# Kernel tuning notes

Measured on AMD Instinct MI355X. Metric: run time of the kernel, lower is better.

Reference implementation:

```python
import jax, jax.numpy as jnp
import numpy as np

N_NODES = 170000
N_EDGES = 1200000
IN, HID, OUT = 128, 128, 64


def setup_inputs() -> dict:
    key = jax.random.key(0)
    ks = jax.random.split(key, 9)
    feat = jax.random.normal(ks[0], (N_NODES, IN), dtype=jnp.float32)
    src = jax.random.randint(ks[1], (N_EDGES,), 0, N_NODES, dtype=jnp.int32)
    dst = jax.random.randint(ks[2], (N_EDGES,), 0, N_NODES, dtype=jnp.int32)
    # Glorot-uniform style init for the GraphConv weights, zero bias (DGL default)
    def glorot(k, fan_in, fan_out):
        lim = np.sqrt(6.0 / (fan_in + fan_out)).astype(np.float32)
        return jax.random.uniform(k, (fan_in, fan_out), jnp.float32, -lim, lim)
    W0 = glorot(ks[3], IN, HID)
    W1 = glorot(ks[4], HID, HID)
    W2 = glorot(ks[5], HID, OUT)
    b0 = jnp.zeros((HID,), jnp.float32)
    b1 = jnp.zeros((HID,), jnp.float32)
    b2 = jnp.zeros((OUT,), jnp.float32)
    return {"feat": feat, "src": src, "dst": dst,
            "W0": W0, "b0": b0, "W1": W1, "b1": b1, "W2": W2, "b2": b2}


def _gcn_layer(h, src, dst, norm_out, norm_in, W, b, relu):
    # norm='both': D_out^{-1/2} scaling, sum-aggregate over edges, D_in^{-1/2} scaling
    h = h * norm_out                                   # [N, d]
    agg = jax.ops.segment_sum(h[src], dst, num_segments=N_NODES)  # gather+scatter-add
    r = (agg * norm_in) @ W + b                        # dense transform + bias
    return jax.nn.relu(r) if relu else r


def reference(feat, src, dst, W0, b0, W1, b1, W2, b2):
    ones = jnp.ones((N_EDGES,), jnp.float32)
    # DGL clamps degrees to min 1 (allow_zero_in_degree=True keeps zero-degree nodes)
    deg_out = jnp.clip(jax.ops.segment_sum(ones, src, num_segments=N_NODES), 1.0)
    deg_in = jnp.clip(jax.ops.segment_sum(ones, dst, num_segments=N_NODES), 1.0)
    norm_out = (deg_out ** -0.5)[:, None]
    norm_in = (deg_in ** -0.5)[:, None]
    # Dropout(0.5) between layers is identity in eval mode
    h = _gcn_layer(feat, src, dst, norm_out, norm_in, W0, b0, relu=True)
    h = _gcn_layer(h, src, dst, norm_out, norm_in, W1, b1, relu=True)
    h = _gcn_layer(h, src, dst, norm_out, norm_in, W2, b2, relu=False)
    return h
```

## Files before the change

kernel.cpp:

```cpp
#include <hip/hip_runtime.h>
#include <hip/hip_bf16.h>

#define N_NODES 170000
#define N_EDGES 1200000

#define AITEMS 2048
#define NB_A   586
#define NCB    333
#define SCAN_A_N      (NCB * NB_A)
#define SCAN_A_BLOCKS 191
#define SCAN_A_PAD    (SCAN_A_BLOCKS * 1024)
#define HISTA_PAD     195140

#define DOUT_NPC    16384
#define DOUT_WPC    8192
#define DOUT_NCHUNK 11
#define DOUT_NSLICE 96
#define DOUT_SLICE_E (N_EDGES / DOUT_NSLICE)
#define WORDS_N     85000

typedef short bf16x8 __attribute__((ext_vector_type(8)));
typedef float f32x4 __attribute__((ext_vector_type(4)));

__device__ __forceinline__ void bf_split(float v, __hip_bfloat16& h, __hip_bfloat16& l)
{
    h = __float2bfloat16(v);
    l = __float2bfloat16(v - __bfloat162float(h));
}


__global__ __launch_bounds__(256) void coarse_hist_kernel(
    const int* __restrict__ dst, int* __restrict__ histA, int nedges)
{
    __shared__ int h[NCB];
    int t = threadIdx.x;
    for (int j = t; j < NCB; j += 256) h[j] = 0;
    __syncthreads();
    int base = blockIdx.x * AITEMS;
    #pragma unroll
    for (int j = 0; j < AITEMS / 256; j++) {
        int i = base + j * 256 + t;
        if (i < nedges) atomicAdd(&h[dst[i] >> 9], 1);
    }
    __syncthreads();
    for (int j = t; j < NCB; j += 256)
        histA[j * NB_A + blockIdx.x] = h[j];
}

__global__ __launch_bounds__(256) void scan1_kernel(
    const int* __restrict__ in, int* __restrict__ partial,
    int* __restrict__ blockSums, int n)
{
    __shared__ int sdata[256];
    int t = threadIdx.x;
    int base = blockIdx.x * 1024 + t * 4;
    int4 v = make_int4(0, 0, 0, 0);
    if (base + 3 < n) v = *(const int4*)&in[base];
    else {
        if (base + 0 < n) v.x = in[base + 0];
        if (base + 1 < n) v.y = in[base + 1];
        if (base + 2 < n) v.z = in[base + 2];
        if (base + 3 < n) v.w = in[base + 3];
    }
    int tsum = v.x + v.y + v.z + v.w;
    sdata[t] = tsum;
    __syncthreads();
    for (int off = 1; off < 256; off <<= 1) {
        int add = 0;
        if (t >= off) add = sdata[t - off];
        __syncthreads();
        if (t >= off) sdata[t] += add;
        __syncthreads();
    }
    int excl = sdata[t] - tsum;
    int4 o;
    o.x = excl;
    o.y = o.x + v.x;
    o.z = o.y + v.y;
    o.w = o.z + v.z;
    *(int4*)&partial[base] = o;
    if (t == 255) blockSums[blockIdx.x] = sdata[255];
}

__global__ __launch_bounds__(256) void scan2_kernel(int* __restrict__ blockSums, int nb)
{
    __shared__ int sdata[256];
    int t = threadIdx.x;
    int val = (t < nb) ? blockSums[t] : 0;
    sdata[t] = val;
    __syncthreads();
    for (int off = 1; off < 256; off <<= 1) {
        int add = 0;
        if (t >= off) add = sdata[t - off];
        __syncthreads();
        if (t >= off) sdata[t] += add;
        __syncthreads();
    }
    if (t < nb) blockSums[t] = sdata[t] - val;
}

__global__ __launch_bounds__(256) void scan3_kernel(
    int* __restrict__ buf, const int* __restrict__ blockSums)
{
    int off = blockSums[blockIdx.x];
    int base = blockIdx.x * 1024 + threadIdx.x * 4;
    int4 v = *(const int4*)&buf[base];
    v.x += off; v.y += off; v.z += off; v.w += off;
    *(int4*)&buf[base] = v;
}

__global__ __launch_bounds__(256) void coarse_scatter_kernel(
    const int* __restrict__ src, const int* __restrict__ dst,
    const int* __restrict__ scanA, int* __restrict__ pairs, int nedges)
{
    __shared__ int base[NCB];
    __shared__ int cur[NCB];
    int t = threadIdx.x;
    for (int j = t; j < NCB; j += 256) {
        base[j] = scanA[j * NB_A + blockIdx.x];
        cur[j] = 0;
    }
    __syncthreads();
    int eb = blockIdx.x * AITEMS;
    #pragma unroll
    for (int j = 0; j < AITEMS / 256; j++) {
        int i = eb + j * 256 + t;
        if (i < nedges) {
            int d = dst[i];
            int cb = d >> 9;
            int r = atomicAdd(&cur[cb], 1);
            pairs[base[cb] + r] = (src[i] << 9) | (d & 511);
        }
    }
}

__global__ __launch_bounds__(256) void bucket_sort_kernel(
    const int* __restrict__ pairs, const int* __restrict__ scanA,
    int* __restrict__ csr, int* __restrict__ row_start,
    float* __restrict__ norm_in, int nedges)
{
    __shared__ int hist[512];
    __shared__ int curs[512];
    __shared__ int sdata[256];
    int cb = blockIdx.x;
    int t = threadIdx.x;
    int beg = scanA[cb * NB_A];
    int end = (cb == NCB - 1) ? nedges : scanA[(cb + 1) * NB_A];

    hist[t] = 0; hist[t + 256] = 0;
    __syncthreads();
    for (int j = beg + t; j < end; j += 256)
        atomicAdd(&hist[pairs[j] & 511], 1);
    __syncthreads();

    int a = hist[2 * t], b = hist[2 * t + 1];
    sdata[t] = a + b;
    __syncthreads();
    for (int off = 1; off < 256; off <<= 1) {
        int add = 0;
        if (t >= off) add = sdata[t - off];
        __syncthreads();
        if (t >= off) sdata[t] += add;
        __syncthreads();
    }
    int epair = sdata[t] - (a + b);
    curs[2 * t]     = beg + epair;
    curs[2 * t + 1] = beg + epair + a;
    __syncthreads();

    int nodeBase = cb << 9;
    for (int s = t; s < 512; s += 256) {
        int v = nodeBase + s;
        if (v < N_NODES) {
            row_start[v] = curs[s];
            norm_in[v] = rsqrtf(fmaxf((float)hist[s], 1.0f));
        }
    }
    if (cb == NCB - 1 && t == 0) row_start[N_NODES] = nedges;
    __syncthreads();

    for (int j = beg + t; j < end; j += 256) {
        int p = pairs[j];
        int pos = atomicAdd(&curs[p & 511], 1);
        csr[pos] = p >> 9;
    }
}

__global__ __launch_bounds__(256) void degout_hist_kernel(
    const int* __restrict__ src, unsigned* __restrict__ partial)
{
    __shared__ unsigned h[DOUT_WPC];
    int chunk = blockIdx.x / DOUT_NSLICE;
    int slice = blockIdx.x % DOUT_NSLICE;
    int lo = chunk * DOUT_NPC;
    int t = threadIdx.x;
    #pragma unroll
    for (int j = 0; j < DOUT_WPC / 256; j++) h[j * 256 + t] = 0;
    __syncthreads();
    const int4* sp = (const int4*)(src + slice * DOUT_SLICE_E);
    for (int i = t; i < DOUT_SLICE_E / 4; i += 256) {
        int4 v = sp[i];
        unsigned a = (unsigned)(v.x - lo);
        if (a < DOUT_NPC) atomicAdd(&h[a >> 1], 1u << ((a & 1) * 16));
        a = (unsigned)(v.y - lo);
        if (a < DOUT_NPC) atomicAdd(&h[a >> 1], 1u << ((a & 1) * 16));
        a = (unsigned)(v.z - lo);
        if (a < DOUT_NPC) atomicAdd(&h[a >> 1], 1u << ((a & 1) * 16));
        a = (unsigned)(v.w - lo);
        if (a < DOUT_NPC) atomicAdd(&h[a >> 1], 1u << ((a & 1) * 16));
    }
    __syncthreads();
    int wlo = chunk * DOUT_WPC;
    int nw = min(DOUT_WPC, WORDS_N - wlo);
    for (int j = t; j < nw; j += 256)
        partial[(size_t)slice * WORDS_N + wlo + j] = h[j];
}

__global__ __launch_bounds__(256) void degout_combine_kernel(
    const unsigned* __restrict__ partial, float* __restrict__ norm_out)
{
    int w = blockIdx.x * 256 + threadIdx.x;
    if (w >= WORDS_N) return;
    unsigned slo = 0, shi = 0;
    #pragma unroll
    for (int s = 0; s < DOUT_NSLICE; s++) {
        unsigned x = partial[(size_t)s * WORDS_N + w];
        slo += x & 0xFFFFu;
        shi += x >> 16;
    }
    norm_out[2 * w]     = rsqrtf(fmaxf((float)slo, 1.0f));
    norm_out[2 * w + 1] = rsqrtf(fmaxf((float)shi, 1.0f));
}

__global__ __launch_bounds__(256) void f2bf_kernel(
    const float* __restrict__ in, __hip_bfloat16* __restrict__ outp, int n8)
{
    int i = blockIdx.x * 256 + threadIdx.x;
    if (i >= n8) return;
    float4 a = *(const float4*)&in[(size_t)i * 8];
    float4 b = *(const float4*)&in[(size_t)i * 8 + 4];
    float4 packed;
    __hip_bfloat162* p = (__hip_bfloat162*)&packed;
    p[0].x = __float2bfloat16(a.x); p[0].y = __float2bfloat16(a.y);
    p[1].x = __float2bfloat16(a.z); p[1].y = __float2bfloat16(a.w);
    p[2].x = __float2bfloat16(b.x); p[2].y = __float2bfloat16(b.y);
    p[3].x = __float2bfloat16(b.z); p[3].y = __float2bfloat16(b.w);
    *(float4*)&outp[(size_t)i * 8] = packed;
}

__global__ __launch_bounds__(256) void wsplit_kernel(
    const float* __restrict__ W, int nout,
    __hip_bfloat16* __restrict__ Whi, __hip_bfloat16* __restrict__ Wlo)
{
    int i = blockIdx.x * 256 + threadIdx.x;
    if (i >= 128 * nout) return;
    int k = i / nout, n = i - k * nout;
    float v = W[i];
    __hip_bfloat16 h, l;
    bf_split(v, h, l);
    Whi[n * 128 + k] = h;
    Wlo[n * 128 + k] = l;
}

template<int W, bool SCALE_SRC, bool SPLIT_OUT, bool BIAS>
__global__ __launch_bounds__(256) void gather_kernel(
    const __hip_bfloat16* __restrict__ h, const int* __restrict__ csr,
    const int* __restrict__ row_start, const float* __restrict__ norm_out,
    const float* __restrict__ norm_in, const float* __restrict__ bias,
    float* __restrict__ outf, __hip_bfloat16* __restrict__ ohi,
    __hip_bfloat16* __restrict__ olo)
{
    int tid = blockIdx.x * 256 + threadIdx.x;
    int row = tid >> 4;
    int l = threadIdx.x & 15;
    int gbase = threadIdx.x & 48;
    if (row >= N_NODES) return;
    int beg = row_start[row];
    int end = row_start[row + 1];
    float acc[8] = {};
    for (int j = beg; j < end; j += 16) {
        int cnt = min(16, end - j);
        int sv = 0;
        float nv = 0.f;
        if (j + l < end) {
            sv = csr[j + l];
            if (SCALE_SRC) nv = norm_out[sv];
        }
        for (int i = 0; i < cnt; i++) {
            int s = __shfl(sv, gbase + i);
            if (W == 128) {
                float4 raw = *(const float4*)(h + (size_t)s * 128 + l * 8);
                const __hip_bfloat162* pp = (const __hip_bfloat162*)&raw;
                float2 f0 = __bfloat1622float2(pp[0]);
                float2 f1 = __bfloat1622float2(pp[1]);
                float2 f2 = __bfloat1622float2(pp[2]);
                float2 f3 = __bfloat1622float2(pp[3]);
                if (SCALE_SRC) {
                    float sc = __shfl(nv, gbase + i);
                    acc[0] += f0.x * sc; acc[1] += f0.y * sc;
                    acc[2] += f1.x * sc; acc[3] += f1.y * sc;
                    acc[4] += f2.x * sc; acc[5] += f2.y * sc;
                    acc[6] += f3.x * sc; acc[7] += f3.y * sc;
                } else {
                    acc[0] += f0.x; acc[1] += f0.y;
                    acc[2] += f1.x; acc[3] += f1.y;
                    acc[4] += f2.x; acc[5] += f2.y;
                    acc[6] += f3.x; acc[7] += f3.y;
                }
            } else {
                float2 raw = *(const float2*)(h + (size_t)s * 64 + l * 4);
                const __hip_bfloat162* pp = (const __hip_bfloat162*)&raw;
                float2 f0 = __bfloat1622float2(pp[0]);
                float2 f1 = __bfloat1622float2(pp[1]);
                acc[0] += f0.x; acc[1] += f0.y;
                acc[2] += f1.x; acc[3] += f1.y;
            }
        }
    }
    float ni = norm_in[row];
    if (W == 128 && SPLIT_OUT) {
        float4 ph, pl;
        __hip_bfloat16* hp = (__hip_bfloat16*)&ph;
        __hip_bfloat16* lp = (__hip_bfloat16*)&pl;
        #pragma unroll
        for (int j = 0; j < 8; j++) bf_split(acc[j] * ni, hp[j], lp[j]);
        *(float4*)(ohi + (size_t)row * 128 + l * 8) = ph;
        *(float4*)(olo + (size_t)row * 128 + l * 8) = pl;
    } else if (W == 64) {
        float4 o0 = make_float4(acc[0] * ni, acc[1] * ni, acc[2] * ni, acc[3] * ni);
        if (BIAS) {
            float4 b = *(const float4*)&bias[l * 4];
            o0.x += b.x; o0.y += b.y; o0.z += b.z; o0.w += b.w;
        }
        *(float4*)&outf[(size_t)row * 64 + l * 4] = o0;
    }
}

template<int NT, bool RELU, bool BIAS, bool RS, bool SPLIT_OUT>
__global__ __launch_bounds__(256) void mfma_matmul_kernel(
    const __hip_bfloat16* __restrict__ Ahi, const __hip_bfloat16* __restrict__ Alo,
    const __hip_bfloat16* __restrict__ Wthi, const __hip_bfloat16* __restrict__ Wtlo,
    const float* __restrict__ bias, const float* __restrict__ rowscale,
    __hip_bfloat16* __restrict__ outhi, __hip_bfloat16* __restrict__ outlo,
    int nrows)
{
    const int OUTW = NT * 16;
    const int wave = threadIdx.x >> 6;
    const int lane = threadIdx.x & 63;
    const int n = lane & 15;
    const int q = lane >> 4;
    const int r0 = blockIdx.x * 128 + wave * 32;
    if (r0 >= nrows) return;
    const bool t1 = (r0 + 16) < nrows;
    const size_t a0off = (size_t)(r0 + n) * 128 + q * 8;
    const size_t a1off = (size_t)(t1 ? (r0 + 16 + n) : (r0 + n)) * 128 + q * 8;
    const size_t bbase = (size_t)n * 128 + q * 8;

    f32x4 acc0[NT], acc1[NT];
    const f32x4 zero = {0.f, 0.f, 0.f, 0.f};
    #pragma unroll
    for (int ct = 0; ct < NT; ct++) { acc0[ct] = zero; acc1[ct] = zero; }

    #pragma unroll 1
    for (int kc = 0; kc < 4; kc++) {
        bf16x8 ah0 = *(const bf16x8*)(Ahi + a0off + kc * 32);
        bf16x8 al0 = *(const bf16x8*)(Alo + a0off + kc * 32);
        bf16x8 ah1 = *(const bf16x8*)(Ahi + a1off + kc * 32);
        bf16x8 al1 = *(const bf16x8*)(Alo + a1off + kc * 32);
        #pragma unroll
        for (int ct = 0; ct < NT; ct++) {
            bf16x8 bh = *(const bf16x8*)(Wthi + (size_t)ct * 2048 + bbase + kc * 32);
            bf16x8 bl = *(const bf16x8*)(Wtlo + (size_t)ct * 2048 + bbase + kc * 32);
            acc0[ct] = __builtin_amdgcn_mfma_f32_16x16x32_bf16(ah0, bh, acc0[ct], 0, 0, 0);
            acc0[ct] = __builtin_amdgcn_mfma_f32_16x16x32_bf16(al0, bh, acc0[ct], 0, 0, 0);
            acc0[ct] = __builtin_amdgcn_mfma_f32_16x16x32_bf16(ah0, bl, acc0[ct], 0, 0, 0);
            acc1[ct] = __builtin_amdgcn_mfma_f32_16x16x32_bf16(ah1, bh, acc1[ct], 0, 0, 0);
            acc1[ct] = __builtin_amdgcn_mfma_f32_16x16x32_bf16(al1, bh, acc1[ct], 0, 0, 0);
            acc1[ct] = __builtin_amdgcn_mfma_f32_16x16x32_bf16(ah1, bl, acc1[ct], 0, 0, 0);
        }
    }

    float bcol[NT];
    #pragma unroll
    for (int ct = 0; ct < NT; ct++) bcol[ct] = BIAS ? bias[ct * 16 + n] : 0.f;

    #pragma unroll
    for (int r = 0; r < 4; r++) {
        int grow = r0 + q * 4 + r;
        float rs = RS ? rowscale[grow] : 1.f;
        #pragma unroll
        for (int ct = 0; ct < NT; ct++) {
            float v = acc0[ct][r] + bcol[ct];
            if (RELU) v = fmaxf(v, 0.f);
            v *= rs;
            size_t o = (size_t)grow * OUTW + ct * 16 + n;
            if (SPLIT_OUT) {
                __hip_bfloat16 h, l;
                bf_split(v, h, l);
                outhi[o] = h; outlo[o] = l;
            } else {
                outhi[o] = __float2bfloat16(v);
            }
        }
    }
    if (t1) {
        #pragma unroll
        for (int r = 0; r < 4; r++) {
            int grow = r0 + 16 + q * 4 + r;
            float rs = RS ? rowscale[grow] : 1.f;
            #pragma unroll
            for (int ct = 0; ct < NT; ct++) {
                float v = acc1[ct][r] + bcol[ct];
                if (RELU) v = fmaxf(v, 0.f);
                v *= rs;
                size_t o = (size_t)grow * OUTW + ct * 16 + n;
                if (SPLIT_OUT) {
                    __hip_bfloat16 h, l;
                    bf_split(v, h, l);
                    outhi[o] = h; outlo[o] = l;
                } else {
                    outhi[o] = __float2bfloat16(v);
                }
            }
        }
    }
}

extern "C" void kernel_launch(void* const* d_in, const int* in_sizes, int n_in,
                              void* d_out, int out_size, void* d_ws, size_t ws_size,
                              hipStream_t stream)
{
    const float* feat = (const float*)d_in[0];
    const int* src    = (const int*)d_in[1];
    const int* dst    = (const int*)d_in[2];
    const float* W0   = (const float*)d_in[3];
    const float* b0   = (const float*)d_in[4];
    const float* W1   = (const float*)d_in[5];
    const float* b1   = (const float*)d_in[6];
    const float* W2   = (const float*)d_in[7];
    const float* b2   = (const float*)d_in[8];
    float* out = (float*)d_out;

    const int N = N_NODES;
    const int E = N_EDGES;

    char* ws = (char*)d_ws;
    float* norm_out = (float*)ws;
    float* norm_in  = norm_out + N;
    int* row_start  = (int*)(norm_in + N);
    int* csr        = row_start + 170004;
    __hip_bfloat16* Wt0hi = (__hip_bfloat16*)(csr + E);
    __hip_bfloat16* Wt0lo = Wt0hi + 16384;
    __hip_bfloat16* Wt1hi = Wt0lo + 16384;
    __hip_bfloat16* Wt1lo = Wt1hi + 16384;
    __hip_bfloat16* Wt2hi = Wt1lo + 16384;
    __hip_bfloat16* Wt2lo = Wt2hi + 8192;
    __hip_bfloat16* bfbuf = Wt2lo + 8192;
    __hip_bfloat16* Ahi   = bfbuf + (size_t)N * 128;
    __hip_bfloat16* Alo   = Ahi + (size_t)N * 128;
    int* histA          = (int*)Ahi;
    int* scanA          = histA + HISTA_PAD;
    int* blockSumsA     = scanA + SCAN_A_PAD + 4;
    unsigned* partial   = (unsigned*)(blockSumsA + 256);
    int* pairs          = (int*)Alo;

    degout_hist_kernel<<<DOUT_NCHUNK * DOUT_NSLICE, 256, 0, stream>>>(src, partial);
    degout_combine_kernel<<<(WORDS_N + 255) / 256, 256, 0, stream>>>(partial, norm_out);
    coarse_hist_kernel<<<NB_A, 256, 0, stream>>>(dst, histA, E);
    scan1_kernel<<<SCAN_A_BLOCKS, 256, 0, stream>>>(histA, scanA, blockSumsA, SCAN_A_N);
    scan2_kernel<<<1, 256, 0, stream>>>(blockSumsA, SCAN_A_BLOCKS);
    scan3_kernel<<<SCAN_A_BLOCKS, 256, 0, stream>>>(scanA, blockSumsA);
    coarse_scatter_kernel<<<NB_A, 256, 0, stream>>>(src, dst, scanA, pairs, E);
    bucket_sort_kernel<<<NCB, 256, 0, stream>>>(pairs, scanA, csr, row_start, norm_in, E);
    f2bf_kernel<<<(N * 16 + 255) / 256, 256, 0, stream>>>(feat, bfbuf, N * 16);
    wsplit_kernel<<<64, 256, 0, stream>>>(W0, 128, Wt0hi, Wt0lo);
    wsplit_kernel<<<64, 256, 0, stream>>>(W1, 128, Wt1hi, Wt1lo);
    wsplit_kernel<<<32, 256, 0, stream>>>(W2, 64, Wt2hi, Wt2lo);

    const int gatherBlocks = (N * 16 + 255) / 256;
    const int mmBlocks = (N + 127) / 128;

    gather_kernel<128, true, true, false><<<gatherBlocks, 256, 0, stream>>>(
        bfbuf, csr, row_start, norm_out, norm_in, nullptr, nullptr, Ahi, Alo);
    mfma_matmul_kernel<8, true, true, true, false><<<mmBlocks, 256, 0, stream>>>(
        Ahi, Alo, Wt0hi, Wt0lo, b0, norm_out, bfbuf, nullptr, N);

    gather_kernel<128, false, true, false><<<gatherBlocks, 256, 0, stream>>>(
        bfbuf, csr, row_start, nullptr, norm_in, nullptr, nullptr, Ahi, Alo);
    mfma_matmul_kernel<8, true, true, true, true><<<mmBlocks, 256, 0, stream>>>(
        Ahi, Alo, Wt1hi, Wt1lo, b1, norm_out, Ahi, Alo, N);

    mfma_matmul_kernel<4, false, false, false, false><<<mmBlocks, 256, 0, stream>>>(
        Ahi, Alo, Wt2hi, Wt2lo, nullptr, nullptr, bfbuf, nullptr, N);
    gather_kernel<64, false, false, true><<<gatherBlocks, 256, 0, stream>>>(
        bfbuf, csr, row_start, nullptr, norm_in, b2, out, nullptr, nullptr);
}
```

Baseline: 638.1 us.

## Fuse neighbor gather with MFMA transform per layer via swizzled LDS tiles

Introduces a fused kernel in which each 32-row block gathers and aggregates its neighbor features, writes the hi/lo bf16 split into swizzled shared memory, and runs the MFMA weight multiply from LDS. The second layer also applies the W2 projection in the same kernel. This removes the global round trips of the split Ahi/Alo intermediates and two kernel launches. In exchange each block holds 16KB of LDS and must finish its gather before the matmul starts, which may reduce occupancy and latency hiding. Weight tiles are now re-read per 32-row block rather than per 128 rows.

New measurement: 518.7 us. 18.7% less time.

```diff
diff --git a/kernel.cpp b/kernel.cpp
--- a/kernel.cpp
+++ b/kernel.cpp
@@ -26,6 +26,11 @@
 {
     h = __float2bfloat16(v);
     l = __float2bfloat16(v - __bfloat162float(h));
+}
+
+__device__ __forceinline__ int lds_addr(int row, int col)
+{
+    return (row * 256 + col * 2) ^ ((row & 7) << 4);
 }
 
 
@@ -260,6 +265,177 @@
     bf_split(v, h, l);
     Whi[n * 128 + k] = h;
     Wlo[n * 128 + k] = l;
+}
+
+template<bool SCALE_SRC, bool FUSE2>
+__global__ __launch_bounds__(256) void fused_layer_kernel(
+    const __hip_bfloat16* __restrict__ hin, const int* __restrict__ csr,
+    const int* __restrict__ row_start, const float* __restrict__ norm_out,
+    const float* __restrict__ norm_in, const __hip_bfloat16* __restrict__ Wthi,
+    const __hip_bfloat16* __restrict__ Wtlo, const float* __restrict__ bias,
+    const float* __restrict__ rowscale, const __hip_bfloat16* __restrict__ W2thi,
+    const __hip_bfloat16* __restrict__ W2tlo, __hip_bfloat16* __restrict__ outp)
+{
+    __shared__ __align__(16) unsigned char smem[16384];
+    const int r0 = blockIdx.x * 32;
+
+    {
+        const int g = threadIdx.x >> 4;
+        const int l = threadIdx.x & 15;
+        const int gbase = threadIdx.x & 48;
+        for (int rr = 0; rr < 2; rr++) {
+            const int lrow = g + rr * 16;
+            const int row = r0 + lrow;
+            float acc[8] = {};
+            if (row < N_NODES) {
+                int beg = row_start[row];
+                int end = row_start[row + 1];
+                for (int j = beg; j < end; j += 16) {
+                    int cnt = min(16, end - j);
+                    int sv = 0;
+                    float nv = 0.f;
+                    if (j + l < end) {
+                        sv = csr[j + l];
+                        if (SCALE_SRC) nv = norm_out[sv];
+                    }
+                    for (int i = 0; i < cnt; i++) {
+                        int s = __shfl(sv, gbase + i);
+                        float4 raw = *(const float4*)(hin + (size_t)s * 128 + l * 8);
+                        const __hip_bfloat162* pp = (const __hip_bfloat162*)&raw;
+                        float2 f0 = __bfloat1622float2(pp[0]);
+                        float2 f1 = __bfloat1622float2(pp[1]);
+                        float2 f2 = __bfloat1622float2(pp[2]);
+                        float2 f3 = __bfloat1622float2(pp[3]);
+                        if (SCALE_SRC) {
+                            float sc = __shfl(nv, gbase + i);
+                            acc[0] += f0.x * sc; acc[1] += f0.y * sc;
+                            acc[2] += f1.x * sc; acc[3] += f1.y * sc;
+                            acc[4] += f2.x * sc; acc[5] += f2.y * sc;
+                            acc[6] += f3.x * sc; acc[7] += f3.y * sc;
+                        } else {
+                            acc[0] += f0.x; acc[1] += f0.y;
+                            acc[2] += f1.x; acc[3] += f1.y;
+                            acc[4] += f2.x; acc[5] += f2.y;
+                            acc[6] += f3.x; acc[7] += f3.y;
+                        }
+                    }
+                }
+            }
+            float ni = (row < N_NODES) ? norm_in[row] : 0.f;
+            float4 ph, pl;
+            __hip_bfloat16* hp = (__hip_bfloat16*)&ph;
+            __hip_bfloat16* lp = (__hip_bfloat16*)&pl;
+            #pragma unroll
+            for (int jj = 0; jj < 8; jj++) bf_split(acc[jj] * ni, hp[jj], lp[jj]);
+            int off = lds_addr(lrow, l * 8);
+            *(float4*)(smem + off) = ph;
+            *(float4*)(smem + 8192 + off) = pl;
+        }
+    }
+    __syncthreads();
+
+    const int wave = threadIdx.x >> 6;
+    const int lane = threadIdx.x & 63;
+    const int n = lane & 15;
+    const int q = lane >> 4;
+    const size_t bbase = (size_t)n * 128 + q * 8;
+    const f32x4 zero = {0.f, 0.f, 0.f, 0.f};
+    f32x4 acc0[2], acc1[2];
+    acc0[0] = zero; acc0[1] = zero; acc1[0] = zero; acc1[1] = zero;
+
+    #pragma unroll 1
+    for (int kc = 0; kc < 4; kc++) {
+        const int a0 = lds_addr(n, q * 8 + kc * 32);
+        const int a1 = lds_addr(n + 16, q * 8 + kc * 32);
+        bf16x8 ah0 = *(const bf16x8*)(smem + a0);
+        bf16x8 al0 = *(const bf16x8*)(smem + 8192 + a0);
+        bf16x8 ah1 = *(const bf16x8*)(smem + a1);
+        bf16x8 al1 = *(const bf16x8*)(smem + 8192 + a1);
+        #pragma unroll
+        for (int c = 0; c < 2; c++) {
+            const int ct = wave * 2 + c;
+            bf16x8 bh = *(const bf16x8*)(Wthi + (size_t)ct * 2048 + bbase + kc * 32);
+            bf16x8 bl = *(const bf16x8*)(Wtlo + (size_t)ct * 2048 + bbase + kc * 32);
+            acc0[c] = __builtin_amdgcn_mfma_f32_16x16x32_bf16(ah0, bh, acc0[c], 0, 0, 0);
+            acc0[c] = __builtin_amdgcn_mfma_f32_16x16x32_bf16(al0, bh, acc0[c], 0, 0, 0);
+            acc0[c] = __builtin_amdgcn_mfma_f32_16x16x32_bf16(ah0, bl, acc0[c], 0, 0, 0);
+            acc1[c] = __builtin_amdgcn_mfma_f32_16x16x32_bf16(ah1, bh, acc1[c], 0, 0, 0);
+            acc1[c] = __builtin_amdgcn_mfma_f32_16x16x32_bf16(al1, bh, acc1[c], 0, 0, 0);
+            acc1[c] = __builtin_amdgcn_mfma_f32_16x16x32_bf16(ah1, bl, acc1[c], 0, 0, 0);
+        }
+    }
+
+    float bcol[2];
+    bcol[0] = bias[(wave * 2 + 0) * 16 + n];
+    bcol[1] = bias[(wave * 2 + 1) * 16 + n];
+
+    if (!FUSE2) {
+        #pragma unroll
+        for (int r = 0; r < 4; r++) {
+            int g0 = r0 + q * 4 + r;
+            int g1 = g0 + 16;
+            float rs0 = rowscale[min(g0, N_NODES - 1)];
+            float rs1 = rowscale[min(g1, N_NODES - 1)];
+            #pragma unroll
+            for (int c = 0; c < 2; c++) {
+                int col = (wave * 2 + c) * 16 + n;
+                float v0 = fmaxf(acc0[c][r] + bcol[c], 0.f) * rs0;
+                float v1 = fmaxf(acc1[c][r] + bcol[c], 0.f) * rs1;
+                if (g0 < N_NODES) outp[(size_t)g0 * 128 + col] = __float2bfloat16(v0);
+                if (g1 < N_NODES) outp[(size_t)g1 * 128 + col] = __float2bfloat16(v1);
+            }
+        }
+    } else {
+        __syncthreads();
+        #pragma unroll
+        for (int r = 0; r < 4; r++) {
+            int lr0 = q * 4 + r;
+            int lr1 = lr0 + 16;
+            float rs0 = rowscale[min(r0 + lr0, N_NODES - 1)];
+            float rs1 = rowscale[min(r0 + lr1, N_NODES - 1)];
+            #pragma unroll
+            for (int c = 0; c < 2; c++) {
+                int col = (wave * 2 + c) * 16 + n;
+                float v0 = fmaxf(acc0[c][r] + bcol[c], 0.f) * rs0;
+                float v1 = fmaxf(acc1[c][r] + bcol[c], 0.f) * rs1;
+                __hip_bfloat16 hh, ll;
+                bf_split(v0, hh, ll);
+                *(__hip_bfloat16*)(smem + lds_addr(lr0, col)) = hh;
+                *(__hip_bfloat16*)(smem + 8192 + lds_addr(lr0, col)) = ll;
+                bf_split(v1, hh, ll);
+                *(__hip_bfloat16*)(smem + lds_addr(lr1, col)) = hh;
+                *(__hip_bfloat16*)(smem + 8192 + lds_addr(lr1, col)) = ll;
+            }
+        }
+        __syncthreads();
+
+        f32x4 c0 = zero, c1 = zero;
+        #pragma unroll 1
+        for (int kc = 0; kc < 4; kc++) {
+            const int a0 = lds_addr(n, q * 8 + kc * 32);
+            const int a1 = lds_addr(n + 16, q * 8 + kc * 32);
+            bf16x8 ah0 = *(const bf16x8*)(smem + a0);
+            bf16x8 al0 = *(const bf16x8*)(smem + 8192 + a0);
+            bf16x8 ah1 = *(const bf16x8*)(smem + a1);
+            bf16x8 al1 = *(const bf16x8*)(smem + 8192 + a1);
+            bf16x8 bh = *(const bf16x8*)(W2thi + (size_t)wave * 2048 + bbase + kc * 32);
+            bf16x8 bl = *(const bf16x8*)(W2tlo + (size_t)wave * 2048 + bbase + kc * 32);
+            c0 = __builtin_amdgcn_mfma_f32_16x16x32_bf16(ah0, bh, c0, 0, 0, 0);
+            c0 = __builtin_amdgcn_mfma_f32_16x16x32_bf16(al0, bh, c0, 0, 0, 0);
+            c0 = __builtin_amdgcn_mfma_f32_16x16x32_bf16(ah0, bl, c0, 0, 0, 0);
+            c1 = __builtin_amdgcn_mfma_f32_16x16x32_bf16(ah1, bh, c1, 0, 0, 0);
+            c1 = __builtin_amdgcn_mfma_f32_16x16x32_bf16(al1, bh, c1, 0, 0, 0);
+            c1 = __builtin_amdgcn_mfma_f32_16x16x32_bf16(ah1, bl, c1, 0, 0, 0);
+        }
+        #pragma unroll
+        for (int r = 0; r < 4; r++) {
+            int g0 = r0 + q * 4 + r;
+            int g1 = g0 + 16;
+            int col = wave * 16 + n;
+            if (g0 < N_NODES) outp[(size_t)g0 * 64 + col] = __float2bfloat16(c0[r]);
+            if (g1 < N_NODES) outp[(size_t)g1 * 64 + col] = __float2bfloat16(c1[r]);
+        }
+    }
 }
 
 template<int W, bool SCALE_SRC, bool SPLIT_OUT, bool BIAS>
@@ -336,96 +512,6 @@
     }
 }
 
-template<int NT, bool RELU, bool BIAS, bool RS, bool SPLIT_OUT>
-__global__ __launch_bounds__(256) void mfma_matmul_kernel(
-    const __hip_bfloat16* __restrict__ Ahi, const __hip_bfloat16* __restrict__ Alo,
-    const __hip_bfloat16* __restrict__ Wthi, const __hip_bfloat16* __restrict__ Wtlo,
-    const float* __restrict__ bias, const float* __restrict__ rowscale,
-    __hip_bfloat16* __restrict__ outhi, __hip_bfloat16* __restrict__ outlo,
-    int nrows)
-{
-    const int OUTW = NT * 16;
-    const int wave = threadIdx.x >> 6;
-    const int lane = threadIdx.x & 63;
-    const int n = lane & 15;
-    const int q = lane >> 4;
-    const int r0 = blockIdx.x * 128 + wave * 32;
-    if (r0 >= nrows) return;
-    const bool t1 = (r0 + 16) < nrows;
-    const size_t a0off = (size_t)(r0 + n) * 128 + q * 8;
-    const size_t a1off = (size_t)(t1 ? (r0 + 16 + n) : (r0 + n)) * 128 + q * 8;
-    const size_t bbase = (size_t)n * 128 + q * 8;
-
-    f32x4 acc0[NT], acc1[NT];
-    const f32x4 zero = {0.f, 0.f, 0.f, 0.f};
-    #pragma unroll
-    for (int ct = 0; ct < NT; ct++) { acc0[ct] = zero; acc1[ct] = zero; }
-
-    #pragma unroll 1
-    for (int kc = 0; kc < 4; kc++) {
-        bf16x8 ah0 = *(const bf16x8*)(Ahi + a0off + kc * 32);
-        bf16x8 al0 = *(const bf16x8*)(Alo + a0off + kc * 32);
-        bf16x8 ah1 = *(const bf16x8*)(Ahi + a1off + kc * 32);
-        bf16x8 al1 = *(const bf16x8*)(Alo + a1off + kc * 32);
-        #pragma unroll
-        for (int ct = 0; ct < NT; ct++) {
-            bf16x8 bh = *(const bf16x8*)(Wthi + (size_t)ct * 2048 + bbase + kc * 32);
-            bf16x8 bl = *(const bf16x8*)(Wtlo + (size_t)ct * 2048 + bbase + kc * 32);
-            acc0[ct] = __builtin_amdgcn_mfma_f32_16x16x32_bf16(ah0, bh, acc0[ct], 0, 0, 0);
-            acc0[ct] = __builtin_amdgcn_mfma_f32_16x16x32_bf16(al0, bh, acc0[ct], 0, 0, 0);
-            acc0[ct] = __builtin_amdgcn_mfma_f32_16x16x32_bf16(ah0, bl, acc0[ct], 0, 0, 0);
-            acc1[ct] = __builtin_amdgcn_mfma_f32_16x16x32_bf16(ah1, bh, acc1[ct], 0, 0, 0);
-            acc1[ct] = __builtin_amdgcn_mfma_f32_16x16x32_bf16(al1, bh, acc1[ct], 0, 0, 0);
-            acc1[ct] = __builtin_amdgcn_mfma_f32_16x16x32_bf16(ah1, bl, acc1[ct], 0, 0, 0);
-        }
-    }
-
-    float bcol[NT];
-    #pragma unroll
-    for (int ct = 0; ct < NT; ct++) bcol[ct] = BIAS ? bias[ct * 16 + n] : 0.f;
-
-    #pragma unroll
-    for (int r = 0; r < 4; r++) {
-        int grow = r0 + q * 4 + r;
-        float rs = RS ? rowscale[grow] : 1.f;
-        #pragma unroll
-        for (int ct = 0; ct < NT; ct++) {
-            float v = acc0[ct][r] + bcol[ct];
-            if (RELU) v = fmaxf(v, 0.f);
-            v *= rs;
-            size_t o = (size_t)grow * OUTW + ct * 16 + n;
-            if (SPLIT_OUT) {
-                __hip_bfloat16 h, l;
-                bf_split(v, h, l);
-                outhi[o] = h; outlo[o] = l;
-            } else {
-                outhi[o] = __float2bfloat16(v);
-            }
-        }
-    }
-    if (t1) {
-        #pragma unroll
-        for (int r = 0; r < 4; r++) {
-            int grow = r0 + 16 + q * 4 + r;
-            float rs = RS ? rowscale[grow] : 1.f;
-            #pragma unroll
-            for (int ct = 0; ct < NT; ct++) {
-                float v = acc1[ct][r] + bcol[ct];
-                if (RELU) v = fmaxf(v, 0.f);
-                v *= rs;
-                size_t o = (size_t)grow * OUTW + ct * 16 + n;
-                if (SPLIT_OUT) {
-                    __hip_bfloat16 h, l;
-                    bf_split(v, h, l);
-                    outhi[o] = h; outlo[o] = l;
-                } else {
-                    outhi[o] = __float2bfloat16(v);
-                }
-            }
-        }
-    }
-}
-
 extern "C" void kernel_launch(void* const* d_in, const int* in_sizes, int n_in,
                               void* d_out, int out_size, void* d_ws, size_t ws_size,
                               hipStream_t stream)
@@ -456,13 +542,13 @@
     __hip_bfloat16* Wt2hi = Wt1lo + 16384;
     __hip_bfloat16* Wt2lo = Wt2hi + 8192;
     __hip_bfloat16* bfbuf = Wt2lo + 8192;
-    __hip_bfloat16* Ahi   = bfbuf + (size_t)N * 128;
-    __hip_bfloat16* Alo   = Ahi + (size_t)N * 128;
-    int* histA          = (int*)Ahi;
+    __hip_bfloat16* h1    = bfbuf + (size_t)N * 128;
+    __hip_bfloat16* aux   = h1 + (size_t)N * 128;
+    int* histA          = (int*)h1;
     int* scanA          = histA + HISTA_PAD;
     int* blockSumsA     = scanA + SCAN_A_PAD + 4;
     unsigned* partial   = (unsigned*)(blockSumsA + 256);
-    int* pairs          = (int*)Alo;
+    int* pairs          = (int*)aux;
 
     degout_hist_kernel<<<DOUT_NCHUNK * DOUT_NSLICE, 256, 0, stream>>>(src, partial);
     degout_combine_kernel<<<(WORDS_N + 255) / 256, 256, 0, stream>>>(partial, norm_out);
@@ -477,21 +563,17 @@
     wsplit_kernel<<<64, 256, 0, stream>>>(W1, 128, Wt1hi, Wt1lo);
     wsplit_kernel<<<32, 256, 0, stream>>>(W2, 64, Wt2hi, Wt2lo);
 
+    const int fusedBlocks = (N + 31) / 32;
     const int gatherBlocks = (N * 16 + 255) / 256;
-    const int mmBlocks = (N + 127) / 128;
-
-    gather_kernel<128, true, true, false><<<gatherBlocks, 256, 0, stream>>>(
-        bfbuf, csr, row_start, norm_out, norm_in, nullptr, nullptr, Ahi, Alo);
-    mfma_matmul_kernel<8, true, true, true, false><<<mmBlocks, 256, 0, stream>>>(
-        Ahi, Alo, Wt0hi, Wt0lo, b0, norm_out, bfbuf, nullptr, N);
-
-    gather_kernel<128, false, true, false><<<gatherBlocks, 256, 0, stream>>>(
-        bfbuf, csr, row_start, nullptr, norm_in, nullptr, nullptr, Ahi, Alo);
-    mfma_matmul_kernel<8, true, true, true, true><<<mmBlocks, 256, 0, stream>>>(
-        Ahi, Alo, Wt1hi, Wt1lo, b1, norm_out, Ahi, Alo, N);
-
-    mfma_matmul_kernel<4, false, false, false, false><<<mmBlocks, 256, 0, stream>>>(
-        Ahi, Alo, Wt2hi, Wt2lo, nullptr, nullptr, bfbuf, nullptr, N);
+
+    fused_layer_kernel<true, false><<<fusedBlocks, 256, 0, stream>>>(
+        bfbuf, csr, row_start, norm_out, norm_in, Wt0hi, Wt0lo, b0, norm_out,
+        nullptr, nullptr, h1);
+
+    fused_layer_kernel<false, true><<<fusedBlocks, 256, 0, stream>>>(
+        h1, csr, row_start, nullptr, norm_in, Wt1hi, Wt1lo, b1, norm_out,
+        Wt2hi, Wt2lo, bfbuf);
+
     gather_kernel<64, false, false, true><<<gatherBlocks, 256, 0, stream>>>(
         bfbuf, csr, row_start, nullptr, norm_in, b2, out, nullptr, nullptr);
 }
```

## Reorder each GCN layer to transform-then-aggregate with single-bf16 activations

Applied to the files above, without the earlier changes.

Each layer now multiplies by the weight first and then aggregates over edges, using linearity, with the norm_out row scaling folded into the GEMM epilogue. Bias and ReLU move into the gather epilogue. Activations are kept as a single bf16 copy instead of a hi/lo split, which removes the extra A loads and one MFMA per pair. The gather loop is also unrolled to issue eight row loads before accumulating, to raise memory-level parallelism. Storing the aggregated input in plain bf16 costs some precision compared with the earlier split representation.

Measured after the change: 573.2 us. -10.2%, faster.

```diff
diff --git a/kernel.cpp b/kernel.cpp
--- a/kernel.cpp
+++ b/kernel.cpp
@@ -262,13 +262,74 @@
     Wlo[n * 128 + k] = l;
 }
 
-template<int W, bool SCALE_SRC, bool SPLIT_OUT, bool BIAS>
-__global__ __launch_bounds__(256) void gather_kernel(
-    const __hip_bfloat16* __restrict__ h, const int* __restrict__ csr,
-    const int* __restrict__ row_start, const float* __restrict__ norm_out,
-    const float* __restrict__ norm_in, const float* __restrict__ bias,
-    float* __restrict__ outf, __hip_bfloat16* __restrict__ ohi,
-    __hip_bfloat16* __restrict__ olo)
+
+template<int NT, bool RS>
+__global__ __launch_bounds__(256) void gemm_kernel(
+    const __hip_bfloat16* __restrict__ A,
+    const __hip_bfloat16* __restrict__ Wthi, const __hip_bfloat16* __restrict__ Wtlo,
+    const float* __restrict__ rowscale, __hip_bfloat16* __restrict__ outp,
+    int nrows)
+{
+    const int OUTW = NT * 16;
+    const int wave = threadIdx.x >> 6;
+    const int lane = threadIdx.x & 63;
+    const int n = lane & 15;
+    const int q = lane >> 4;
+    const int r0 = blockIdx.x * 128 + wave * 32;
+    if (r0 >= nrows) return;
+    const bool t1 = (r0 + 16) < nrows;
+    const size_t a0off = (size_t)(r0 + n) * 128 + q * 8;
+    const size_t a1off = (size_t)(t1 ? (r0 + 16 + n) : (r0 + n)) * 128 + q * 8;
+    const size_t bbase = (size_t)n * 128 + q * 8;
+
+    f32x4 acc0[NT], acc1[NT];
+    const f32x4 zero = {0.f, 0.f, 0.f, 0.f};
+    #pragma unroll
+    for (int ct = 0; ct < NT; ct++) { acc0[ct] = zero; acc1[ct] = zero; }
+
+    #pragma unroll 1
+    for (int kc = 0; kc < 4; kc++) {
+        bf16x8 ah0 = *(const bf16x8*)(A + a0off + kc * 32);
+        bf16x8 ah1 = *(const bf16x8*)(A + a1off + kc * 32);
+        #pragma unroll
+        for (int ct = 0; ct < NT; ct++) {
+            bf16x8 bh = *(const bf16x8*)(Wthi + (size_t)ct * 2048 + bbase + kc * 32);
+            bf16x8 bl = *(const bf16x8*)(Wtlo + (size_t)ct * 2048 + bbase + kc * 32);
+            acc0[ct] = __builtin_amdgcn_mfma_f32_16x16x32_bf16(ah0, bh, acc0[ct], 0, 0, 0);
+            acc0[ct] = __builtin_amdgcn_mfma_f32_16x16x32_bf16(ah0, bl, acc0[ct], 0, 0, 0);
+            acc1[ct] = __builtin_amdgcn_mfma_f32_16x16x32_bf16(ah1, bh, acc1[ct], 0, 0, 0);
+            acc1[ct] = __builtin_amdgcn_mfma_f32_16x16x32_bf16(ah1, bl, acc1[ct], 0, 0, 0);
+        }
+    }
+
+    #pragma unroll
+    for (int r = 0; r < 4; r++) {
+        int grow = r0 + q * 4 + r;
+        float rs = RS ? rowscale[grow] : 1.f;
+        #pragma unroll
+        for (int ct = 0; ct < NT; ct++) {
+            float v = acc0[ct][r] * rs;
+            outp[(size_t)grow * OUTW + ct * 16 + n] = __float2bfloat16(v);
+        }
+    }
+    if (t1) {
+        #pragma unroll
+        for (int r = 0; r < 4; r++) {
+            int grow = r0 + 16 + q * 4 + r;
+            float rs = RS ? rowscale[grow] : 1.f;
+            #pragma unroll
+            for (int ct = 0; ct < NT; ct++) {
+                float v = acc1[ct][r] * rs;
+                outp[(size_t)grow * OUTW + ct * 16 + n] = __float2bfloat16(v);
+            }
+        }
+    }
+}
+
+__global__ __launch_bounds__(256) void gather128_kernel(
+    const __hip_bfloat16* __restrict__ t, const int* __restrict__ csr,
+    const int* __restrict__ row_start, const float* __restrict__ norm_in,
+    const float* __restrict__ bias, __hip_bfloat16* __restrict__ outp)
 {
     int tid = blockIdx.x * 256 + threadIdx.x;
     int row = tid >> 4;
@@ -281,149 +342,97 @@
     for (int j = beg; j < end; j += 16) {
         int cnt = min(16, end - j);
         int sv = 0;
-        float nv = 0.f;
-        if (j + l < end) {
-            sv = csr[j + l];
-            if (SCALE_SRC) nv = norm_out[sv];
-        }
-        for (int i = 0; i < cnt; i++) {
-            int s = __shfl(sv, gbase + i);
-            if (W == 128) {
-                float4 raw = *(const float4*)(h + (size_t)s * 128 + l * 8);
-                const __hip_bfloat162* pp = (const __hip_bfloat162*)&raw;
-                float2 f0 = __bfloat1622float2(pp[0]);
-                float2 f1 = __bfloat1622float2(pp[1]);
-                float2 f2 = __bfloat1622float2(pp[2]);
-                float2 f3 = __bfloat1622float2(pp[3]);
-                if (SCALE_SRC) {
-                    float sc = __shfl(nv, gbase + i);
+        float wv = 0.f;
+        if (j + l < end) { sv = csr[j + l]; wv = 1.f; }
+        int s0 = __shfl(sv, gbase);
+        if (j + l >= end) sv = s0;
+        #pragma unroll
+        for (int ib = 0; ib < 16; ib += 8) {
+            if (ib < cnt) {
+                float4 rg[8];
+                float ww[8];
+                #pragma unroll
+                for (int k = 0; k < 8; k++) {
+                    int s = __shfl(sv, gbase + ib + k);
+                    ww[k] = __shfl(wv, gbase + ib + k);
+                    rg[k] = *(const float4*)(t + (size_t)s * 128 + l * 8);
+                }
+                #pragma unroll
+                for (int k = 0; k < 8; k++) {
+                    const __hip_bfloat162* pp = (const __hip_bfloat162*)&rg[k];
+                    float sc = ww[k];
+                    float2 f0 = __bfloat1622float2(pp[0]);
+                    float2 f1 = __bfloat1622float2(pp[1]);
+                    float2 f2 = __bfloat1622float2(pp[2]);
+                    float2 f3 = __bfloat1622float2(pp[3]);
                     acc[0] += f0.x * sc; acc[1] += f0.y * sc;
                     acc[2] += f1.x * sc; acc[3] += f1.y * sc;
                     acc[4] += f2.x * sc; acc[5] += f2.y * sc;
                     acc[6] += f3.x * sc; acc[7] += f3.y * sc;
-                } else {
-                    acc[0] += f0.x; acc[1] += f0.y;
-                    acc[2] += f1.x; acc[3] += f1.y;
-                    acc[4] += f2.x; acc[5] += f2.y;
-                    acc[6] += f3.x; acc[7] += f3.y;
-                }
-            } else {
-                float2 raw = *(const float2*)(h + (size_t)s * 64 + l * 4);
-                const __hip_bfloat162* pp = (const __hip_bfloat162*)&raw;
-                float2 f0 = __bfloat1622float2(pp[0]);
-                float2 f1 = __bfloat1622float2(pp[1]);
-                acc[0] += f0.x; acc[1] += f0.y;
-                acc[2] += f1.x; acc[3] += f1.y;
-            }
-        }
-    }
-    float ni = norm_in[row];
-    if (W == 128 && SPLIT_OUT) {
-        float4 ph, pl;
-        __hip_bfloat16* hp = (__hip_bfloat16*)&ph;
-        __hip_bfloat16* lp = (__hip_bfloat16*)&pl;
-        #pragma unroll
-        for (int j = 0; j < 8; j++) bf_split(acc[j] * ni, hp[j], lp[j]);
-        *(float4*)(ohi + (size_t)row * 128 + l * 8) = ph;
-        *(float4*)(olo + (size_t)row * 128 + l * 8) = pl;
-    } else if (W == 64) {
-        float4 o0 = make_float4(acc[0] * ni, acc[1] * ni, acc[2] * ni, acc[3] * ni);
-        if (BIAS) {
-            float4 b = *(const float4*)&bias[l * 4];
-            o0.x += b.x; o0.y += b.y; o0.z += b.z; o0.w += b.w;
-        }
-        *(float4*)&outf[(size_t)row * 64 + l * 4] = o0;
-    }
-}
-
-template<int NT, bool RELU, bool BIAS, bool RS, bool SPLIT_OUT>
-__global__ __launch_bounds__(256) void mfma_matmul_kernel(
-    const __hip_bfloat16* __restrict__ Ahi, const __hip_bfloat16* __restrict__ Alo,
-    const __hip_bfloat16* __restrict__ Wthi, const __hip_bfloat16* __restrict__ Wtlo,
-    const float* __restrict__ bias, const float* __restrict__ rowscale,
-    __hip_bfloat16* __restrict__ outhi, __hip_bfloat16* __restrict__ outlo,
-    int nrows)
-{
-    const int OUTW = NT * 16;
-    const int wave = threadIdx.x >> 6;
-    const int lane = threadIdx.x & 63;
-    const int n = lane & 15;
-    const int q = lane >> 4;
-    const int r0 = blockIdx.x * 128 + wave * 32;
-    if (r0 >= nrows) return;
-    const bool t1 = (r0 + 16) < nrows;
-    const size_t a0off = (size_t)(r0 + n) * 128 + q * 8;
-    const size_t a1off = (size_t)(t1 ? (r0 + 16 + n) : (r0 + n)) * 128 + q * 8;
-    const size_t bbase = (size_t)n * 128 + q * 8;
-
-    f32x4 acc0[NT], acc1[NT];
-    const f32x4 zero = {0.f, 0.f, 0.f, 0.f};
-    #pragma unroll
-    for (int ct = 0; ct < NT; ct++) { acc0[ct] = zero; acc1[ct] = zero; }
-
-    #pragma unroll 1
-    for (int kc = 0; kc < 4; kc++) {
-        bf16x8 ah0 = *(const bf16x8*)(Ahi + a0off + kc * 32);
-        bf16x8 al0 = *(const bf16x8*)(Alo + a0off + kc * 32);
-        bf16x8 ah1 = *(const bf16x8*)(Ahi + a1off + kc * 32);
-        bf16x8 al1 = *(const bf16x8*)(Alo + a1off + kc * 32);
-        #pragma unroll
-        for (int ct = 0; ct < NT; ct++) {
-            bf16x8 bh = *(const bf16x8*)(Wthi + (size_t)ct * 2048 + bbase + kc * 32);
-            bf16x8 bl = *(const bf16x8*)(Wtlo + (size_t)ct * 2048 + bbase + kc * 32);
-            acc0[ct] = __builtin_amdgcn_mfma_f32_16x16x32_bf16(ah0, bh, acc0[ct], 0, 0, 0);
-            acc0[ct] = __builtin_amdgcn_mfma_f32_16x16x32_bf16(al0, bh, acc0[ct], 0, 0, 0);
-            acc0[ct] = __builtin_amdgcn_mfma_f32_16x16x32_bf16(ah0, bl, acc0[ct], 0, 0, 0);
-            acc1[ct] = __builtin_amdgcn_mfma_f32_16x16x32_bf16(ah1, bh, acc1[ct], 0, 0, 0);
-            acc1[ct] = __builtin_amdgcn_mfma_f32_16x16x32_bf16(al1, bh, acc1[ct], 0, 0, 0);
-            acc1[ct] = __builtin_amdgcn_mfma_f32_16x16x32_bf16(ah1, bl, acc1[ct], 0, 0, 0);
-        }
-    }
-
-    float bcol[NT];
-    #pragma unroll
-    for (int ct = 0; ct < NT; ct++) bcol[ct] = BIAS ? bias[ct * 16 + n] : 0.f;
-
-    #pragma unroll
-    for (int r = 0; r < 4; r++) {
-        int grow = r0 + q * 4 + r;
-        float rs = RS ? rowscale[grow] : 1.f;
-        #pragma unroll
-        for (int ct = 0; ct < NT; ct++) {
-            float v = acc0[ct][r] + bcol[ct];
-            if (RELU) v = fmaxf(v, 0.f);
-            v *= rs;
-            size_t o = (size_t)grow * OUTW + ct * 16 + n;
-            if (SPLIT_OUT) {
-                __hip_bfloat16 h, l;
-                bf_split(v, h, l);
-                outhi[o] = h; outlo[o] = l;
-            } else {
-                outhi[o] = __float2bfloat16(v);
-            }
-        }
-    }
-    if (t1) {
-        #pragma unroll
-        for (int r = 0; r < 4; r++) {
-            int grow = r0 + 16 + q * 4 + r;
-            float rs = RS ? rowscale[grow] : 1.f;
-            #pragma unroll
-            for (int ct = 0; ct < NT; ct++) {
-                float v = acc1[ct][r] + bcol[ct];
-                if (RELU) v = fmaxf(v, 0.f);
-                v *= rs;
-                size_t o = (size_t)grow * OUTW + ct * 16 + n;
-                if (SPLIT_OUT) {
-                    __hip_bfloat16 h, l;
-                    bf_split(v, h, l);
-                    outhi[o] = h; outlo[o] = l;
-                } else {
-                    outhi[o] = __float2bfloat16(v);
                 }
             }
         }
     }
+    float ni = norm_in[row];
+    float4 b0 = *(const float4*)&bias[l * 8];
+    float4 b1 = *(const float4*)&bias[l * 8 + 4];
+    float bb[8] = {b0.x, b0.y, b0.z, b0.w, b1.x, b1.y, b1.z, b1.w};
+    float4 packed;
+    __hip_bfloat16* hp = (__hip_bfloat16*)&packed;
+    #pragma unroll
+    for (int k = 0; k < 8; k++)
+        hp[k] = __float2bfloat16(fmaxf(acc[k] * ni + bb[k], 0.f));
+    *(float4*)(outp + (size_t)row * 128 + l * 8) = packed;
+}
+
+__global__ __launch_bounds__(256) void final_gather_kernel(
+    const __hip_bfloat16* __restrict__ h, const int* __restrict__ csr,
+    const int* __restrict__ row_start, const float* __restrict__ norm_in,
+    const float* __restrict__ bias, float* __restrict__ outf)
+{
+    int tid = blockIdx.x * 256 + threadIdx.x;
+    int row = tid >> 4;
+    int l = threadIdx.x & 15;
+    int gbase = threadIdx.x & 48;
+    if (row >= N_NODES) return;
+    int beg = row_start[row];
+    int end = row_start[row + 1];
+    float acc[4] = {};
+    for (int j = beg; j < end; j += 16) {
+        int cnt = min(16, end - j);
+        int sv = 0;
+        float wv = 0.f;
+        if (j + l < end) { sv = csr[j + l]; wv = 1.f; }
+        int s0 = __shfl(sv, gbase);
+        if (j + l >= end) sv = s0;
+        #pragma unroll
+        for (int ib = 0; ib < 16; ib += 8) {
+            if (ib < cnt) {
+                float2 rg[8];
+                float ww[8];
+                #pragma unroll
+                for (int k = 0; k < 8; k++) {
+                    int s = __shfl(sv, gbase + ib + k);
+                    ww[k] = __shfl(wv, gbase + ib + k);
+                    rg[k] = *(const float2*)(h + (size_t)s * 64 + l * 4);
+                }
+                #pragma unroll
+                for (int k = 0; k < 8; k++) {
+                    const __hip_bfloat162* pp = (const __hip_bfloat162*)&rg[k];
+                    float sc = ww[k];
+                    float2 f0 = __bfloat1622float2(pp[0]);
+                    float2 f1 = __bfloat1622float2(pp[1]);
+                    acc[0] += f0.x * sc; acc[1] += f0.y * sc;
+                    acc[2] += f1.x * sc; acc[3] += f1.y * sc;
+                }
+            }
+        }
+    }
+    float ni = norm_in[row];
+    float4 o0 = make_float4(acc[0] * ni, acc[1] * ni, acc[2] * ni, acc[3] * ni);
+    float4 b = *(const float4*)&bias[l * 4];
+    o0.x += b.x; o0.y += b.y; o0.z += b.z; o0.w += b.w;
+    *(float4*)&outf[(size_t)row * 64 + l * 4] = o0;
 }
 
 extern "C" void kernel_launch(void* const* d_in, const int* in_sizes, int n_in,
@@ -455,14 +464,14 @@
     __hip_bfloat16* Wt1lo = Wt1hi + 16384;
     __hip_bfloat16* Wt2hi = Wt1lo + 16384;
     __hip_bfloat16* Wt2lo = Wt2hi + 8192;
-    __hip_bfloat16* bfbuf = Wt2lo + 8192;
-    __hip_bfloat16* Ahi   = bfbuf + (size_t)N * 128;
-    __hip_bfloat16* Alo   = Ahi + (size_t)N * 128;
-    int* histA          = (int*)Ahi;
+    __hip_bfloat16* P0 = Wt2lo + 8192;
+    __hip_bfloat16* P1 = P0 + (size_t)N * 128;
+    __hip_bfloat16* aux = P1 + (size_t)N * 128;
+    int* histA          = (int*)P1;
     int* scanA          = histA + HISTA_PAD;
     int* blockSumsA     = scanA + SCAN_A_PAD + 4;
     unsigned* partial   = (unsigned*)(blockSumsA + 256);
-    int* pairs          = (int*)Alo;
+    int* pairs          = (int*)aux;
 
     degout_hist_kernel<<<DOUT_NCHUNK * DOUT_NSLICE, 256, 0, stream>>>(src, partial);
     degout_combine_kernel<<<(WORDS_N + 255) / 256, 256, 0, stream>>>(partial, norm_out);
@@ -472,26 +481,20 @@
     scan3_kernel<<<SCAN_A_BLOCKS, 256, 0, stream>>>(scanA, blockSumsA);
     coarse_scatter_kernel<<<NB_A, 256, 0, stream>>>(src, dst, scanA, pairs, E);
     bucket_sort_kernel<<<NCB, 256, 0, stream>>>(pairs, scanA, csr, row_start, norm_in, E);
-    f2bf_kernel<<<(N * 16 + 255) / 256, 256, 0, stream>>>(feat, bfbuf, N * 16);
+    f2bf_kernel<<<(N * 16 + 255) / 256, 256, 0, stream>>>(feat, P0, N * 16);
     wsplit_kernel<<<64, 256, 0, stream>>>(W0, 128, Wt0hi, Wt0lo);
     wsplit_kernel<<<64, 256, 0, stream>>>(W1, 128, Wt1hi, Wt1lo);
     wsplit_kernel<<<32, 256, 0, stream>>>(W2, 64, Wt2hi, Wt2lo);
 
+    const int mmBlocks = (N + 127) / 128;
     const int gatherBlocks = (N * 16 + 255) / 256;
-    const int mmBlocks = (N + 127) / 128;
-
-    gather_kernel<128, true, true, false><<<gatherBlocks, 256, 0, stream>>>(
-        bfbuf, csr, row_start, norm_out, norm_in, nullptr, nullptr, Ahi, Alo);
-    mfma_matmul_kernel<8, true, true, true, false><<<mmBlocks, 256, 0, stream>>>(
-        Ahi, Alo, Wt0hi, Wt0lo, b0, norm_out, bfbuf, nullptr, N);
-
-    gather_kernel<128, false, true, false><<<gatherBlocks, 256, 0, stream>>>(
-        bfbuf, csr, row_start, nullptr, norm_in, nullptr, nullptr, Ahi, Alo);
-    mfma_matmul_kernel<8, true, true, true, true><<<mmBlocks, 256, 0, stream>>>(
-        Ahi, Alo, Wt1hi, Wt1lo, b1, norm_out, Ahi, Alo, N);
-
-    mfma_matmul_kernel<4, false, false, false, false><<<mmBlocks, 256, 0, stream>>>(
-        Ahi, Alo, Wt2hi, Wt2lo, nullptr, nullptr, bfbuf, nullptr, N);
-    gather_kernel<64, false, false, true><<<gatherBlocks, 256, 0, stream>>>(
-        bfbuf, csr, row_start, nullptr, norm_in, b2, out, nullptr, nullptr);
-}
+
+    gemm_kernel<8, true><<<mmBlocks, 256, 0, stream>>>(P0, Wt0hi, Wt0lo, norm_out, P1, N);
+    gather128_kernel<<<gatherBlocks, 256, 0, stream>>>(P1, csr, row_start, norm_in, b0, P0);
+
+    gemm_kernel<8, true><<<mmBlocks, 256, 0, stream>>>(P0, Wt1hi, Wt1lo, norm_out, P1, N);
+    gather128_kernel<<<gatherBlocks, 256, 0, stream>>>(P1, csr, row_start, norm_in, b1, P0);
+
+    gemm_kernel<4, true><<<mmBlocks, 256, 0, stream>>>(P0, Wt2hi, Wt2lo, norm_out, P1, N);
+    final_gather_kernel<<<gatherBlocks, 256, 0, stream>>>(P1, csr, row_start, norm_in, b2, out);
+}
```
